# Performance work log

Hardware: AMD Instinct MI355X
Metric: run time of the kernel (lower is better)

The kernel has to match this reference:

```python
import jax, jax.numpy as jnp
import numpy as np

B, S, D_IN, D_OUT, N_EXPERTS = 8, 4096, 512, 512, 8


def setup_inputs() -> dict:
    key = jax.random.key(0)
    k1, k2, k3, k4 = jax.random.split(key, 4)
    x = jax.random.normal(k1, (B, S, D_IN), dtype=jnp.float32)
    partitions = jax.random.randint(k2, (B, S), 0, N_EXPERTS, dtype=jnp.int32)
    # per-branch nn.Linear weights: [n, out_features, in_features], kaiming-ish scale
    W = jax.random.normal(k3, (N_EXPERTS, D_OUT, D_IN), dtype=jnp.float32) * 0.03
    b = jax.random.normal(k4, (N_EXPERTS, D_OUT), dtype=jnp.float32) * 0.01
    return {"x": x, "partitions": partitions, "W": W, "b": b}


def reference(x, partitions, W, b):
    # Hard token partition -> per-branch linear -> scatter combine.
    # Equivalent math to dynamic_partition + branch Linear + dynamic_stitch:
    # out[t] = x[t] @ W[p[t]].T + b[p[t]]
    in_shape = x.shape
    xf = x.reshape(-1, in_shape[-1])          # [T, d_in]
    p = partitions.reshape(-1)                # [T]
    # Compute all-expert outputs, then select per-token expert (vectorized
    # replacement for the variable-size per-partition GEMM loop).
    y = jnp.einsum('td,eod->teo', xf, W) + b[None, :, :]   # [T, n, d_out]
    out = jnp.take_along_axis(y, p[:, None, None], axis=1)[:, 0, :]  # [T, d_out]
    return out.reshape(in_shape[:-1] + (W.shape[1],))
```

## Files before the change

### kernel.cpp

```cpp
#include <hip/hip_runtime.h>
#include <hip/hip_bf16.h>

#define N_EXPERTS 8
#define T_TOKENS 32768
#define D 512
#define TILE 128
#define BK 64
#define NT 4
#define LT_MAX 256
#define GEMM_GRID (N_EXPERTS * LT_MAX * NT)
#define SCATTER_BLOCKS (T_TOKENS / 256)
#define CONVW_BLOCKS ((N_EXPERTS * D * D) / (8 * 256))
#define CONVX_BLOCKS ((T_TOKENS * D) / (8 * 256))

typedef __bf16 bf16x8 __attribute__((ext_vector_type(8)));
typedef float  f32x4  __attribute__((ext_vector_type(4)));
typedef unsigned short u16x8 __attribute__((ext_vector_type(8)));

__device__ __forceinline__ unsigned short f2bf(float f) {
    unsigned int u = __float_as_uint(f);
    u += 0x7FFFu + ((u >> 16) & 1u);
    return (unsigned short)(u >> 16);
}

__device__ __forceinline__ u16x8 cvt8(float4 a, float4 b) {
    u16x8 o;
    o[0] = f2bf(a.x); o[1] = f2bf(a.y); o[2] = f2bf(a.z); o[3] = f2bf(a.w);
    o[4] = f2bf(b.x); o[5] = f2bf(b.y); o[6] = f2bf(b.z); o[7] = f2bf(b.w);
    return o;
}

__device__ __forceinline__ void gl2lds16(const void* g, void* l) {
    __builtin_amdgcn_global_load_lds(
        (const __attribute__((address_space(1))) void*)g,
        (__attribute__((address_space(3))) void*)l, 16, 0, 0);
}

__global__ __launch_bounds__(256) void prep_kernel(
        const int* __restrict__ p, int* __restrict__ fill, int* __restrict__ sorted,
        const float* __restrict__ W, unsigned short* __restrict__ Wb,
        const float* __restrict__ x, unsigned short* __restrict__ xb) {
    int bid = blockIdx.x;
    int tid = threadIdx.x;
    if (bid < SCATTER_BLOCKS) {
        __shared__ int lcount[N_EXPERTS];
        __shared__ int lbase[N_EXPERTS];
        if (tid < N_EXPERTS) lcount[tid] = 0;
        __syncthreads();
        int t = bid * 256 + tid;
        int e = p[t];
        int lrank = atomicAdd(&lcount[e], 1);
        __syncthreads();
        if (tid < N_EXPERTS)
            lbase[tid] = (lcount[tid] > 0) ? atomicAdd(&fill[tid], lcount[tid]) : 0;
        __syncthreads();
        sorted[e * T_TOKENS + (lbase[e] + 1 + lrank)] = t;
    } else if (bid < SCATTER_BLOCKS + CONVW_BLOCKS) {
        size_t i = ((size_t)(bid - SCATTER_BLOCKS) * 256 + tid) * 8;
        float4 a = *(const float4*)(W + i);
        float4 b = *(const float4*)(W + i + 4);
        *(u16x8*)&Wb[i] = cvt8(a, b);
    } else {
        size_t i = ((size_t)(bid - SCATTER_BLOCKS - CONVW_BLOCKS) * 256 + tid) * 8;
        float4 a = *(const float4*)(x + i);
        float4 b = *(const float4*)(x + i + 4);
        *(u16x8*)&xb[i] = cvt8(a, b);
    }
}

__global__ __launch_bounds__(256, 2) void moe_gemm_dma(
        const unsigned short* __restrict__ xb, const unsigned short* __restrict__ Wb,
        const float* __restrict__ bias, const int* __restrict__ fill,
        const int* __restrict__ sorted, float* __restrict__ out) {
    __shared__ int s_idx[TILE];
    __shared__ unsigned short buf[2][2][TILE * BK];

    int bid = blockIdx.x;
    int e = bid & 7;
    int cnt = fill[e] + 1;
    int j = bid >> 3;
    int lt = j >> 2, bn = j & 3;
    int row0 = lt * TILE;
    if (row0 >= cnt) return;

    int tid = threadIdx.x;
    if (tid < TILE) {
        int r = row0 + tid;
        s_idx[tid] = (r < cnt) ? sorted[e * T_TOKENS + r] : -1;
    }
    __syncthreads();

    int wave = tid >> 6, lane = tid & 63;
    int wm = (wave >> 1) * 64, wn = (wave & 1) * 64;
    int lrow = lane & 15, lq = lane >> 4;
    int srow = lane >> 3, scol = lane & 7, swz = scol ^ srow;

    const unsigned short* gA[4];
#pragma unroll
    for (int t = 0; t < 4; t++) {
        int tok = s_idx[wave * 32 + t * 8 + srow];
        gA[t] = xb + (size_t)(tok < 0 ? 0 : tok) * D + swz * 8;
    }
    const unsigned short* gB = Wb + (size_t)e * D * D
                             + (size_t)(bn * TILE + wave * 32 + srow) * D + swz * 8;

#define STAGE(K, KB) do {                                                     \
    _Pragma("unroll") for (int t = 0; t < 4; t++)                             \
        gl2lds16(gA[t] + (K) * BK, &buf[KB][0][(wave * 32 + t * 8) * BK]);    \
    _Pragma("unroll") for (int t = 0; t < 4; t++)                             \
        gl2lds16(gB + (size_t)(t * 8) * D + (K) * BK,                         \
                 &buf[KB][1][(wave * 32 + t * 8) * BK]);                      \
} while (0)

    f32x4 acc[4][4];
#pragma unroll
    for (int i = 0; i < 4; i++)
#pragma unroll
        for (int j2 = 0; j2 < 4; j2++)
            acc[i][j2] = (f32x4){0.f, 0.f, 0.f, 0.f};

    STAGE(0, 0);

#pragma unroll
    for (int step = 0; step < 8; step++) {
        asm volatile("s_waitcnt lgkmcnt(0)" ::: "memory");
        __builtin_amdgcn_s_barrier();
        __builtin_amdgcn_sched_barrier(0);
        if (step < 7) {
            STAGE(step + 1, (step + 1) & 1);
            __builtin_amdgcn_sched_barrier(0);
            asm volatile("s_waitcnt vmcnt(8)" ::: "memory");
        } else {
            asm volatile("s_waitcnt vmcnt(0)" ::: "memory");
        }
        __builtin_amdgcn_s_barrier();
        __builtin_amdgcn_sched_barrier(0);
        const unsigned short* sA = buf[step & 1][0];
        const unsigned short* sB = buf[step & 1][1];
        __builtin_amdgcn_s_setprio(1);
#pragma unroll
        for (int ks = 0; ks < 2; ks++) {
            bf16x8 af[4], bfr[4];
#pragma unroll
            for (int i = 0; i < 4; i++) {
                int row = wm + 16 * i + lrow;
                int cb = (ks * 4 + lq) ^ (lrow & 7);
                af[i] = *(const bf16x8*)&sA[row * BK + cb * 8];
            }
#pragma unroll
            for (int j2 = 0; j2 < 4; j2++) {
                int row = wn + 16 * j2 + lrow;
                int cb = (ks * 4 + lq) ^ (lrow & 7);
                bfr[j2] = *(const bf16x8*)&sB[row * BK + cb * 8];
            }
#pragma unroll
            for (int i = 0; i < 4; i++)
#pragma unroll
                for (int j2 = 0; j2 < 4; j2++)
                    acc[i][j2] = __builtin_amdgcn_mfma_f32_16x16x32_bf16(
                        af[i], bfr[j2], acc[i][j2], 0, 0, 0);
        }
        __builtin_amdgcn_s_setprio(0);
    }
#undef STAGE

#pragma unroll
    for (int j2 = 0; j2 < 4; j2++) {
        float bv = bias[e * D + bn * TILE + wn + 16 * j2 + lrow];
#pragma unroll
        for (int i = 0; i < 4; i++)
#pragma unroll
            for (int r = 0; r < 4; r++)
                acc[i][j2][r] += bv;
    }

    float* ct = (float*)&buf[0][0][0];
#pragma unroll
    for (int p = 0; p < 2; p++) {
        asm volatile("s_waitcnt lgkmcnt(0)" ::: "memory");
        __builtin_amdgcn_s_barrier();
        if ((wave >> 1) == p) {
#pragma unroll
            for (int j2 = 0; j2 < 4; j2++)
#pragma unroll
                for (int i = 0; i < 4; i++)
#pragma unroll
                    for (int r = 0; r < 4; r++)
                        ct[(16 * i + lq * 4 + r) * TILE + wn + 16 * j2 + lrow]
                            = acc[i][j2][r];
        }
        asm volatile("s_waitcnt lgkmcnt(0)" ::: "memory");
        __builtin_amdgcn_s_barrier();
#pragma unroll
        for (int k = 0; k < 8; k++) {
            int u = tid + 256 * k;
            int row = u >> 5, ch = u & 31;
            int tok = s_idx[p * 64 + row];
            f32x4 v = *(const f32x4*)&ct[row * TILE + ch * 4];
            if (tok >= 0)
                *(f32x4*)&out[(size_t)tok * D + bn * TILE + ch * 4] = v;
        }
    }
}

__global__ __launch_bounds__(256) void moe_gemm_f32(
        const float* __restrict__ x, const float* __restrict__ W,
        const float* __restrict__ bias, const int* __restrict__ fill,
        const int* __restrict__ sorted, float* __restrict__ out) {
    __shared__ int s_idx[TILE];
    __shared__ unsigned short sA[TILE][BK + 8];
    __shared__ unsigned short sB[TILE][BK + 8];

    int bid = blockIdx.x;
    int e = bid & 7;
    int cnt = fill[e] + 1;
    int j = bid >> 3;
    int lt = j >> 2, bn = j & 3;
    int row0 = lt * TILE;
    if (row0 >= cnt) return;

    int tid = threadIdx.x;
    if (tid < TILE) {
        int r = row0 + tid;
        s_idx[tid] = (r < cnt) ? sorted[e * T_TOKENS + r] : -1;
    }
    __syncthreads();

    const float* Wbp = W + (size_t)e * D * D + (size_t)(bn * TILE) * D;

    f32x4 acc[4][4];
#pragma unroll
    for (int i = 0; i < 4; i++)
#pragma unroll
        for (int j2 = 0; j2 < 4; j2++)
            acc[i][j2] = (f32x4){0.f, 0.f, 0.f, 0.f};

    int wave = tid >> 6, lane = tid & 63;
    int wm = (wave >> 1) * 64, wn = (wave & 1) * 64;
    int lrow = lane & 15, lq = lane >> 4;

    for (int kk = 0; kk < D; kk += BK) {
#pragma unroll
        for (int i = 0; i < 8; i++) {
            int flat = tid + i * 256;
            int r = flat >> 4, c = (flat & 15) << 2;
            int tok = s_idx[r];
            float4 v = make_float4(0.f, 0.f, 0.f, 0.f);
            if (tok >= 0) v = *(const float4*)(x + (size_t)tok * D + kk + c);
            ushort4 w4;
            w4.x = f2bf(v.x); w4.y = f2bf(v.y); w4.z = f2bf(v.z); w4.w = f2bf(v.w);
            *(ushort4*)&sA[r][c] = w4;
        }
#pragma unroll
        for (int i = 0; i < 8; i++) {
            int flat = tid + i * 256;
            int r = flat >> 4, c = (flat & 15) << 2;
            float4 v = *(const float4*)(Wbp + (size_t)r * D + kk + c);
            ushort4 w4;
            w4.x = f2bf(v.x); w4.y = f2bf(v.y); w4.z = f2bf(v.z); w4.w = f2bf(v.w);
            *(ushort4*)&sB[r][c] = w4;
        }
        __syncthreads();
#pragma unroll
        for (int ks = 0; ks < 2; ks++) {
            bf16x8 af[4], bfr[4];
#pragma unroll
            for (int i = 0; i < 4; i++)
                af[i] = *(const bf16x8*)&sA[wm + 16 * i + lrow][ks * 32 + lq * 8];
#pragma unroll
            for (int j2 = 0; j2 < 4; j2++)
                bfr[j2] = *(const bf16x8*)&sB[wn + 16 * j2 + lrow][ks * 32 + lq * 8];
#pragma unroll
            for (int i = 0; i < 4; i++)
#pragma unroll
                for (int j2 = 0; j2 < 4; j2++)
                    acc[i][j2] = __builtin_amdgcn_mfma_f32_16x16x32_bf16(
                        af[i], bfr[j2], acc[i][j2], 0, 0, 0);
        }
        __syncthreads();
    }

#pragma unroll
    for (int j2 = 0; j2 < 4; j2++) {
        int ng = bn * TILE + wn + 16 * j2 + lrow;
        float bv = bias[e * D + ng];
#pragma unroll
        for (int i = 0; i < 4; i++) {
#pragma unroll
            for (int r = 0; r < 4; r++) {
                int mrow = wm + 16 * i + lq * 4 + r;
                int tok = s_idx[mrow];
                if (tok >= 0)
                    out[(size_t)tok * D + ng] = acc[i][j2][r] + bv;
            }
        }
    }
}

extern "C" void kernel_launch(void* const* d_in, const int* in_sizes, int n_in,
                              void* d_out, int out_size, void* d_ws, size_t ws_size,
                              hipStream_t stream) {
    const float* x    = (const float*)d_in[0];
    const int*   part = (const int*)d_in[1];
    const float* W    = (const float*)d_in[2];
    const float* b    = (const float*)d_in[3];
    float* out = (float*)d_out;

    const size_t xb_elems     = (size_t)T_TOKENS * D;
    const size_t wb_elems     = (size_t)N_EXPERTS * D * D;
    const size_t sorted_elems = (size_t)N_EXPERTS * T_TOKENS;
    const size_t fast_bytes   = (xb_elems + wb_elems) * 2 + (sorted_elems + 8) * 4;
    const size_t slow_bytes   = (sorted_elems + 8) * 4;

    if (ws_size >= fast_bytes) {
        unsigned short* xb = (unsigned short*)d_ws;
        unsigned short* Wb = xb + xb_elems;
        int* sorted = (int*)(Wb + wb_elems);
        int* fill   = sorted + sorted_elems;

        hipMemsetAsync(fill, 0xFF, N_EXPERTS * sizeof(int), stream);
        prep_kernel<<<SCATTER_BLOCKS + CONVW_BLOCKS + CONVX_BLOCKS, 256, 0, stream>>>(
            part, fill, sorted, W, Wb, x, xb);
        moe_gemm_dma<<<GEMM_GRID, 256, 0, stream>>>(xb, Wb, b, fill, sorted, out);
    } else if (ws_size >= slow_bytes) {
        int* sorted = (int*)d_ws;
        int* fill   = sorted + sorted_elems;

        hipMemsetAsync(fill, 0xFF, N_EXPERTS * sizeof(int), stream);
        prep_kernel<<<SCATTER_BLOCKS, 256, 0, stream>>>(
            part, fill, sorted, W, (unsigned short*)nullptr,
            x, (unsigned short*)nullptr);
        moe_gemm_f32<<<GEMM_GRID, 256, 0, stream>>>(x, W, b, fill, sorted, out);
    }
}
```

Before: 153.6 us.

## Use 256x256 GEMM tiles with 512 threads and a compact expert-tile grid

Replaces the 128x128 MoE GEMM kernel with a 256x256-tile version run by 512 threads, with each wave computing a 128x64 sub-tile. The old sparse grid launched every possible expert tile and had most blocks exit early; the new grid is compact, and each block finds its expert and local tile by a prefix scan over per-expert tile counts. Larger tiles raise operand reuse and cut redundant loads of A and B. In exchange the kernel needs about 128KB of LDS, which allows only one block per CU, and its roughly 270 blocks on 256 CUs leave a small tail wave.

```diff
diff --git a/kernel.cpp b/kernel.cpp
--- a/kernel.cpp
+++ b/kernel.cpp
@@ -4,11 +4,14 @@
 #define N_EXPERTS 8
 #define T_TOKENS 32768
 #define D 512
+#define BM 256
+#define BN 256
+#define BK 64
+#define MT_MAX 135
+#define GRID2 (MT_MAX * 2)
 #define TILE 128
-#define BK 64
-#define NT 4
 #define LT_MAX 256
-#define GEMM_GRID (N_EXPERTS * LT_MAX * NT)
+#define GEMM_GRID (N_EXPERTS * LT_MAX * 4)
 #define SCATTER_BLOCKS (T_TOKENS / 256)
 #define CONVW_BLOCKS ((N_EXPERTS * D * D) / (8 * 256))
 #define CONVX_BLOCKS ((T_TOKENS * D) / (8 * 256))
@@ -68,30 +71,38 @@
     }
 }
 
-__global__ __launch_bounds__(256, 2) void moe_gemm_dma(
+__global__ __launch_bounds__(512, 2) void moe_gemm_256(
         const unsigned short* __restrict__ xb, const unsigned short* __restrict__ Wb,
         const float* __restrict__ bias, const int* __restrict__ fill,
         const int* __restrict__ sorted, float* __restrict__ out) {
-    __shared__ int s_idx[TILE];
-    __shared__ unsigned short buf[2][2][TILE * BK];
+    __shared__ int s_idx[BM];
+    __shared__ unsigned short smem[4 * BM * BK];
+    unsigned short* sAb = smem;
+    unsigned short* sBb = smem + 2 * BM * BK;
 
     int bid = blockIdx.x;
-    int e = bid & 7;
-    int cnt = fill[e] + 1;
-    int j = bid >> 3;
-    int lt = j >> 2, bn = j & 3;
-    int row0 = lt * TILE;
-    if (row0 >= cnt) return;
+    int bn = bid & 1, m = bid >> 1;
+
+    int e = 0, lt = 0, tacc = 0, found = 0, cnt_e = 0;
+#pragma unroll
+    for (int i = 0; i < N_EXPERTS; i++) {
+        int c = fill[i] + 1;
+        int tiles = (c + BM - 1) >> 8;
+        if (!found && m < tacc + tiles) { e = i; lt = m - tacc; cnt_e = c; found = 1; }
+        tacc += tiles;
+    }
+    if (!found) return;
+    int row0 = lt * BM;
 
     int tid = threadIdx.x;
-    if (tid < TILE) {
+    if (tid < BM) {
         int r = row0 + tid;
-        s_idx[tid] = (r < cnt) ? sorted[e * T_TOKENS + r] : -1;
+        s_idx[tid] = (r < cnt_e) ? sorted[e * T_TOKENS + r] : -1;
     }
     __syncthreads();
 
     int wave = tid >> 6, lane = tid & 63;
-    int wm = (wave >> 1) * 64, wn = (wave & 1) * 64;
+    int wm = (wave >> 2) * 128, wn = (wave & 3) * 64;
     int lrow = lane & 15, lq = lane >> 4;
     int srow = lane >> 3, scol = lane & 7, swz = scol ^ srow;
 
@@ -102,19 +113,20 @@
         gA[t] = xb + (size_t)(tok < 0 ? 0 : tok) * D + swz * 8;
     }
     const unsigned short* gB = Wb + (size_t)e * D * D
-                             + (size_t)(bn * TILE + wave * 32 + srow) * D + swz * 8;
-
-#define STAGE(K, KB) do {                                                     \
-    _Pragma("unroll") for (int t = 0; t < 4; t++)                             \
-        gl2lds16(gA[t] + (K) * BK, &buf[KB][0][(wave * 32 + t * 8) * BK]);    \
-    _Pragma("unroll") for (int t = 0; t < 4; t++)                             \
-        gl2lds16(gB + (size_t)(t * 8) * D + (K) * BK,                         \
-                 &buf[KB][1][(wave * 32 + t * 8) * BK]);                      \
+                             + (size_t)(bn * BN + wave * 32 + srow) * D + swz * 8;
+
+#define STAGE(K, KB) do {                                                       \
+    _Pragma("unroll") for (int t = 0; t < 4; t++)                               \
+        gl2lds16(gA[t] + (K) * BK,                                              \
+                 &sAb[(KB) * BM * BK + (wave * 32 + t * 8) * BK]);              \
+    _Pragma("unroll") for (int t = 0; t < 4; t++)                               \
+        gl2lds16(gB + (size_t)(t * 8) * D + (K) * BK,                           \
+                 &sBb[(KB) * BM * BK + (wave * 32 + t * 8) * BK]);              \
 } while (0)
 
-    f32x4 acc[4][4];
-#pragma unroll
-    for (int i = 0; i < 4; i++)
+    f32x4 acc[8][4];
+#pragma unroll
+    for (int i = 0; i < 8; i++)
 #pragma unroll
         for (int j2 = 0; j2 < 4; j2++)
             acc[i][j2] = (f32x4){0.f, 0.f, 0.f, 0.f};
@@ -135,26 +147,21 @@
         }
         __builtin_amdgcn_s_barrier();
         __builtin_amdgcn_sched_barrier(0);
-        const unsigned short* sA = buf[step & 1][0];
-        const unsigned short* sB = buf[step & 1][1];
+        const unsigned short* cA = sAb + (step & 1) * BM * BK;
+        const unsigned short* cB = sBb + (step & 1) * BM * BK;
         __builtin_amdgcn_s_setprio(1);
 #pragma unroll
         for (int ks = 0; ks < 2; ks++) {
-            bf16x8 af[4], bfr[4];
-#pragma unroll
-            for (int i = 0; i < 4; i++) {
-                int row = wm + 16 * i + lrow;
-                int cb = (ks * 4 + lq) ^ (lrow & 7);
-                af[i] = *(const bf16x8*)&sA[row * BK + cb * 8];
-            }
-#pragma unroll
-            for (int j2 = 0; j2 < 4; j2++) {
-                int row = wn + 16 * j2 + lrow;
-                int cb = (ks * 4 + lq) ^ (lrow & 7);
-                bfr[j2] = *(const bf16x8*)&sB[row * BK + cb * 8];
-            }
-#pragma unroll
-            for (int i = 0; i < 4; i++)
+            int cb = (ks * 4 + lq) ^ (lrow & 7);
+            bf16x8 af[8], bfr[4];
+#pragma unroll
+            for (int i = 0; i < 8; i++)
+                af[i] = *(const bf16x8*)&cA[(wm + 16 * i + lrow) * BK + cb * 8];
+#pragma unroll
+            for (int j2 = 0; j2 < 4; j2++)
+                bfr[j2] = *(const bf16x8*)&cB[(wn + 16 * j2 + lrow) * BK + cb * 8];
+#pragma unroll
+            for (int i = 0; i < 8; i++)
 #pragma unroll
                 for (int j2 = 0; j2 < 4; j2++)
                     acc[i][j2] = __builtin_amdgcn_mfma_f32_16x16x32_bf16(
@@ -166,39 +173,39 @@
 
 #pragma unroll
     for (int j2 = 0; j2 < 4; j2++) {
-        float bv = bias[e * D + bn * TILE + wn + 16 * j2 + lrow];
-#pragma unroll
-        for (int i = 0; i < 4; i++)
+        float bv = bias[e * D + bn * BN + wn + 16 * j2 + lrow];
+#pragma unroll
+        for (int i = 0; i < 8; i++)
 #pragma unroll
             for (int r = 0; r < 4; r++)
                 acc[i][j2][r] += bv;
     }
 
-    float* ct = (float*)&buf[0][0][0];
+    float* ct = (float*)smem;
 #pragma unroll
     for (int p = 0; p < 2; p++) {
         asm volatile("s_waitcnt lgkmcnt(0)" ::: "memory");
         __builtin_amdgcn_s_barrier();
-        if ((wave >> 1) == p) {
-#pragma unroll
-            for (int j2 = 0; j2 < 4; j2++)
-#pragma unroll
-                for (int i = 0; i < 4; i++)
+        if ((wave >> 2) == p) {
+#pragma unroll
+            for (int i = 0; i < 8; i++)
+#pragma unroll
+                for (int j2 = 0; j2 < 4; j2++)
 #pragma unroll
                     for (int r = 0; r < 4; r++)
-                        ct[(16 * i + lq * 4 + r) * TILE + wn + 16 * j2 + lrow]
+                        ct[(16 * i + lq * 4 + r) * BN + wn + 16 * j2 + lrow]
                             = acc[i][j2][r];
         }
         asm volatile("s_waitcnt lgkmcnt(0)" ::: "memory");
         __builtin_amdgcn_s_barrier();
 #pragma unroll
-        for (int k = 0; k < 8; k++) {
-            int u = tid + 256 * k;
-            int row = u >> 5, ch = u & 31;
-            int tok = s_idx[p * 64 + row];
-            f32x4 v = *(const f32x4*)&ct[row * TILE + ch * 4];
+        for (int k = 0; k < 16; k++) {
+            int u = tid + 512 * k;
+            int row = u >> 6, ch = u & 63;
+            int tok = s_idx[p * 128 + row];
+            f32x4 v = *(const f32x4*)&ct[row * BN + ch * 4];
             if (tok >= 0)
-                *(f32x4*)&out[(size_t)tok * D + bn * TILE + ch * 4] = v;
+                *(f32x4*)&out[(size_t)tok * D + bn * BN + ch * 4] = v;
         }
     }
 }
@@ -321,7 +328,7 @@
         hipMemsetAsync(fill, 0xFF, N_EXPERTS * sizeof(int), stream);
         prep_kernel<<<SCATTER_BLOCKS + CONVW_BLOCKS + CONVX_BLOCKS, 256, 0, stream>>>(
             part, fill, sorted, W, Wb, x, xb);
-        moe_gemm_dma<<<GEMM_GRID, 256, 0, stream>>>(xb, Wb, b, fill, sorted, out);
+        moe_gemm_256<<<GRID2, 512, 0, stream>>>(xb, Wb, b, fill, sorted, out);
     } else if (ws_size >= slow_bytes) {
         int* sorted = (int*)d_ws;
         int* fill   = sorted + sorted_elems;
```

Result: slower. 162.4 us (+5.7%).

## Pre-gather tokens into packed swizzled bf16 tiles and compact the GEMM grid

Applied to the files above, without the earlier changes.

Input conversion now happens per expert tile. A new gather kernel reads the sorted token indices and writes each 128-row tile of x as bf16, contiguous and pre-swizzled per K chunk. W is likewise converted into per-(expert, column-block) packed swizzled tiles. The GEMM streams both operands with fully contiguous global-to-LDS loads, and its grid covers only the occupied tiles through a prefix walk over the expert counts, instead of launching 8x256x4 blocks that mostly exit early. The cost is an extra kernel launch and a serial dependency on the scatter result before gathering.

```diff
diff --git a/kernel.cpp b/kernel.cpp
--- a/kernel.cpp
+++ b/kernel.cpp
@@ -6,12 +6,15 @@
 #define D 512
 #define TILE 128
 #define BK 64
-#define NT 4
+#define NKK (D / BK)
+#define CHUNK 8192
+#define TILE_U16 (NKK * CHUNK)
+#define MT_MAX 264
+#define GRID_WG (MT_MAX * 4)
+#define SCATTER_BLOCKS (T_TOKENS / 256)
+#define CONVW_BLOCKS 128
 #define LT_MAX 256
-#define GEMM_GRID (N_EXPERTS * LT_MAX * NT)
-#define SCATTER_BLOCKS (T_TOKENS / 256)
-#define CONVW_BLOCKS ((N_EXPERTS * D * D) / (8 * 256))
-#define CONVX_BLOCKS ((T_TOKENS * D) / (8 * 256))
+#define GEMM_GRID (N_EXPERTS * LT_MAX * 4)
 
 typedef __bf16 bf16x8 __attribute__((ext_vector_type(8)));
 typedef float  f32x4  __attribute__((ext_vector_type(4)));
@@ -36,10 +39,9 @@
         (__attribute__((address_space(3))) void*)l, 16, 0, 0);
 }
 
-__global__ __launch_bounds__(256) void prep_kernel(
+__global__ __launch_bounds__(256) void scatter_convw(
         const int* __restrict__ p, int* __restrict__ fill, int* __restrict__ sorted,
-        const float* __restrict__ W, unsigned short* __restrict__ Wb,
-        const float* __restrict__ x, unsigned short* __restrict__ xb) {
+        const float* __restrict__ W, unsigned short* __restrict__ Wt) {
     int bid = blockIdx.x;
     int tid = threadIdx.x;
     if (bid < SCATTER_BLOCKS) {
@@ -55,61 +57,102 @@
             lbase[tid] = (lcount[tid] > 0) ? atomicAdd(&fill[tid], lcount[tid]) : 0;
         __syncthreads();
         sorted[e * T_TOKENS + (lbase[e] + 1 + lrank)] = t;
-    } else if (bid < SCATTER_BLOCKS + CONVW_BLOCKS) {
-        size_t i = ((size_t)(bid - SCATTER_BLOCKS) * 256 + tid) * 8;
-        float4 a = *(const float4*)(W + i);
-        float4 b = *(const float4*)(W + i + 4);
-        *(u16x8*)&Wb[i] = cvt8(a, b);
     } else {
-        size_t i = ((size_t)(bid - SCATTER_BLOCKS - CONVW_BLOCKS) * 256 + tid) * 8;
-        float4 a = *(const float4*)(x + i);
-        float4 b = *(const float4*)(x + i + 4);
-        *(u16x8*)&xb[i] = cvt8(a, b);
-    }
-}
-
-__global__ __launch_bounds__(256, 2) void moe_gemm_dma(
-        const unsigned short* __restrict__ xb, const unsigned short* __restrict__ Wb,
+        int i2 = bid - SCATTER_BLOCKS;
+        int e = i2 >> 4, bn = (i2 >> 2) & 3, q = i2 & 3;
+        int wave = tid >> 6, lane = tid & 63;
+        int kk = lane >> 3, b = lane & 7;
+        unsigned short* base = Wt + (size_t)(e * 4 + bn) * TILE_U16 + kk * CHUNK;
+#pragma unroll
+        for (int rr = 0; rr < 8; rr++) {
+            int row = q * 32 + wave * 8 + rr;
+            const float* src = W + ((size_t)e * D + bn * TILE + row) * D + lane * 8;
+            float4 a = *(const float4*)src;
+            float4 c = *(const float4*)(src + 4);
+            *(u16x8*)&base[row * 64 + ((b ^ (row & 7)) << 3)] = cvt8(a, c);
+        }
+    }
+}
+
+__global__ __launch_bounds__(256) void gather_pack_x(
+        const float* __restrict__ x, const int* __restrict__ fill,
+        const int* __restrict__ sorted, unsigned short* __restrict__ xs) {
+    int m = blockIdx.x;
+    int e = 0, lt = 0, tacc = 0, found = 0, cnt_e = 0;
+#pragma unroll
+    for (int i = 0; i < N_EXPERTS; i++) {
+        int c = fill[i] + 1;
+        int tiles = (c + TILE - 1) >> 7;
+        if (!found && m < tacc + tiles) { e = i; lt = m - tacc; cnt_e = c; found = 1; }
+        tacc += tiles;
+    }
+    if (!found) return;
+
+    int tid = threadIdx.x, wave = tid >> 6, lane = tid & 63;
+    int kk = lane >> 3, b = lane & 7;
+    unsigned short* base = xs + (size_t)m * TILE_U16 + kk * CHUNK;
+    int row0 = lt * TILE;
+#pragma unroll 4
+    for (int rr = 0; rr < 32; rr++) {
+        int row = wave * 32 + rr;
+        int r = row0 + row;
+        int tok = (r < cnt_e) ? sorted[e * T_TOKENS + r] : -1;
+        u16x8 v = (u16x8)0;
+        if (tok >= 0) {
+            const float* src = x + (size_t)tok * D + lane * 8;
+            float4 a = *(const float4*)src;
+            float4 c = *(const float4*)(src + 4);
+            v = cvt8(a, c);
+        }
+        *(u16x8*)&base[row * 64 + ((b ^ (row & 7)) << 3)] = v;
+    }
+}
+
+__global__ __launch_bounds__(256, 2) void moe_gemm_pk(
+        const unsigned short* __restrict__ xs, const unsigned short* __restrict__ Wt,
         const float* __restrict__ bias, const int* __restrict__ fill,
         const int* __restrict__ sorted, float* __restrict__ out) {
     __shared__ int s_idx[TILE];
-    __shared__ unsigned short buf[2][2][TILE * BK];
+    __shared__ unsigned short sA[2][TILE * BK];
+    __shared__ unsigned short sB[2][TILE * BK];
 
     int bid = blockIdx.x;
-    int e = bid & 7;
-    int cnt = fill[e] + 1;
-    int j = bid >> 3;
-    int lt = j >> 2, bn = j & 3;
+    int w6 = bid >> 3;
+    int m = (bid & 7) + (w6 >> 2) * 8;
+    int bn = w6 & 3;
+
+    int e = 0, lt = 0, tacc = 0, found = 0, cnt_e = 0;
+#pragma unroll
+    for (int i = 0; i < N_EXPERTS; i++) {
+        int c = fill[i] + 1;
+        int tiles = (c + TILE - 1) >> 7;
+        if (!found && m < tacc + tiles) { e = i; lt = m - tacc; cnt_e = c; found = 1; }
+        tacc += tiles;
+    }
+    if (!found) return;
     int row0 = lt * TILE;
-    if (row0 >= cnt) return;
 
     int tid = threadIdx.x;
     if (tid < TILE) {
         int r = row0 + tid;
-        s_idx[tid] = (r < cnt) ? sorted[e * T_TOKENS + r] : -1;
+        s_idx[tid] = (r < cnt_e) ? sorted[e * T_TOKENS + r] : -1;
     }
     __syncthreads();
 
     int wave = tid >> 6, lane = tid & 63;
     int wm = (wave >> 1) * 64, wn = (wave & 1) * 64;
     int lrow = lane & 15, lq = lane >> 4;
-    int srow = lane >> 3, scol = lane & 7, swz = scol ^ srow;
-
-    const unsigned short* gA[4];
-#pragma unroll
-    for (int t = 0; t < 4; t++) {
-        int tok = s_idx[wave * 32 + t * 8 + srow];
-        gA[t] = xb + (size_t)(tok < 0 ? 0 : tok) * D + swz * 8;
-    }
-    const unsigned short* gB = Wb + (size_t)e * D * D
-                             + (size_t)(bn * TILE + wave * 32 + srow) * D + swz * 8;
-
-#define STAGE(K, KB) do {                                                     \
-    _Pragma("unroll") for (int t = 0; t < 4; t++)                             \
-        gl2lds16(gA[t] + (K) * BK, &buf[KB][0][(wave * 32 + t * 8) * BK]);    \
-    _Pragma("unroll") for (int t = 0; t < 4; t++)                             \
-        gl2lds16(gB + (size_t)(t * 8) * D + (K) * BK,                         \
-                 &buf[KB][1][(wave * 32 + t * 8) * BK]);                      \
+
+    const unsigned short* gAc = xs + (size_t)m * TILE_U16;
+    const unsigned short* gBc = Wt + (size_t)(e * 4 + bn) * TILE_U16;
+
+#define STAGE(K, KB) do {                                                      \
+    _Pragma("unroll") for (int t = 0; t < 4; t++)                              \
+        gl2lds16(gAc + (size_t)(K) * CHUNK + (wave * 4 + t) * 512 + lane * 8,  \
+                 &sA[KB][(wave * 4 + t) * 512]);                               \
+    _Pragma("unroll") for (int t = 0; t < 4; t++)                              \
+        gl2lds16(gBc + (size_t)(K) * CHUNK + (wave * 4 + t) * 512 + lane * 8,  \
+                 &sB[KB][(wave * 4 + t) * 512]);                               \
 } while (0)
 
     f32x4 acc[4][4];
@@ -122,11 +165,11 @@
     STAGE(0, 0);
 
 #pragma unroll
-    for (int step = 0; step < 8; step++) {
+    for (int step = 0; step < NKK; step++) {
         asm volatile("s_waitcnt lgkmcnt(0)" ::: "memory");
         __builtin_amdgcn_s_barrier();
         __builtin_amdgcn_sched_barrier(0);
-        if (step < 7) {
+        if (step < NKK - 1) {
             STAGE(step + 1, (step + 1) & 1);
             __builtin_amdgcn_sched_barrier(0);
             asm volatile("s_waitcnt vmcnt(8)" ::: "memory");
@@ -135,24 +178,19 @@
         }
         __builtin_amdgcn_s_barrier();
         __builtin_amdgcn_sched_barrier(0);
-        const unsigned short* sA = buf[step & 1][0];
-        const unsigned short* sB = buf[step & 1][1];
+        const unsigned short* cA = sA[step & 1];
+        const unsigned short* cB = sB[step & 1];
         __builtin_amdgcn_s_setprio(1);
 #pragma unroll
         for (int ks = 0; ks < 2; ks++) {
+            int cb = (ks * 4 + lq) ^ (lrow & 7);
             bf16x8 af[4], bfr[4];
 #pragma unroll
-            for (int i = 0; i < 4; i++) {
-                int row = wm + 16 * i + lrow;
-                int cb = (ks * 4 + lq) ^ (lrow & 7);
-                af[i] = *(const bf16x8*)&sA[row * BK + cb * 8];
-            }
-#pragma unroll
-            for (int j2 = 0; j2 < 4; j2++) {
-                int row = wn + 16 * j2 + lrow;
-                int cb = (ks * 4 + lq) ^ (lrow & 7);
-                bfr[j2] = *(const bf16x8*)&sB[row * BK + cb * 8];
-            }
+            for (int i = 0; i < 4; i++)
+                af[i] = *(const bf16x8*)&cA[(wm + 16 * i + lrow) * BK + cb * 8];
+#pragma unroll
+            for (int j2 = 0; j2 < 4; j2++)
+                bfr[j2] = *(const bf16x8*)&cB[(wn + 16 * j2 + lrow) * BK + cb * 8];
 #pragma unroll
             for (int i = 0; i < 4; i++)
 #pragma unroll
@@ -174,16 +212,16 @@
                 acc[i][j2][r] += bv;
     }
 
-    float* ct = (float*)&buf[0][0][0];
+    float* ct = (float*)&sA[0][0];
 #pragma unroll
     for (int p = 0; p < 2; p++) {
         asm volatile("s_waitcnt lgkmcnt(0)" ::: "memory");
         __builtin_amdgcn_s_barrier();
         if ((wave >> 1) == p) {
 #pragma unroll
-            for (int j2 = 0; j2 < 4; j2++)
-#pragma unroll
-                for (int i = 0; i < 4; i++)
+            for (int i = 0; i < 4; i++)
+#pragma unroll
+                for (int j2 = 0; j2 < 4; j2++)
 #pragma unroll
                     for (int r = 0; r < 4; r++)
                         ct[(16 * i + lq * 4 + r) * TILE + wn + 16 * j2 + lrow]
@@ -306,30 +344,30 @@
     const float* b    = (const float*)d_in[3];
     float* out = (float*)d_out;
 
-    const size_t xb_elems     = (size_t)T_TOKENS * D;
-    const size_t wb_elems     = (size_t)N_EXPERTS * D * D;
+    const size_t xs_elems     = (size_t)MT_MAX * TILE_U16;
+    const size_t wt_elems     = (size_t)N_EXPERTS * 4 * TILE_U16;
     const size_t sorted_elems = (size_t)N_EXPERTS * T_TOKENS;
-    const size_t fast_bytes   = (xb_elems + wb_elems) * 2 + (sorted_elems + 8) * 4;
+    const size_t fast_bytes   = (xs_elems + wt_elems) * 2 + (sorted_elems + 8) * 4;
     const size_t slow_bytes   = (sorted_elems + 8) * 4;
 
     if (ws_size >= fast_bytes) {
-        unsigned short* xb = (unsigned short*)d_ws;
-        unsigned short* Wb = xb + xb_elems;
-        int* sorted = (int*)(Wb + wb_elems);
+        unsigned short* xs = (unsigned short*)d_ws;
+        unsigned short* Wt = xs + xs_elems;
+        int* sorted = (int*)(Wt + wt_elems);
         int* fill   = sorted + sorted_elems;
 
         hipMemsetAsync(fill, 0xFF, N_EXPERTS * sizeof(int), stream);
-        prep_kernel<<<SCATTER_BLOCKS + CONVW_BLOCKS + CONVX_BLOCKS, 256, 0, stream>>>(
-            part, fill, sorted, W, Wb, x, xb);
-        moe_gemm_dma<<<GEMM_GRID, 256, 0, stream>>>(xb, Wb, b, fill, sorted, out);
+        scatter_convw<<<SCATTER_BLOCKS + CONVW_BLOCKS, 256, 0, stream>>>(
+            part, fill, sorted, W, Wt);
+        gather_pack_x<<<MT_MAX, 256, 0, stream>>>(x, fill, sorted, xs);
+        moe_gemm_pk<<<GRID_WG, 256, 0, stream>>>(xs, Wt, b, fill, sorted, out);
     } else if (ws_size >= slow_bytes) {
         int* sorted = (int*)d_ws;
         int* fill   = sorted + sorted_elems;
 
         hipMemsetAsync(fill, 0xFF, N_EXPERTS * sizeof(int), stream);
-        prep_kernel<<<SCATTER_BLOCKS, 256, 0, stream>>>(
-            part, fill, sorted, W, (unsigned short*)nullptr,
-            x, (unsigned short*)nullptr);
+        scatter_convw<<<SCATTER_BLOCKS, 256, 0, stream>>>(
+            part, fill, sorted, (const float*)nullptr, (unsigned short*)nullptr);
         moe_gemm_f32<<<GEMM_GRID, 256, 0, stream>>>(x, W, b, fill, sorted, out);
     }
 }
```

Measured after the change: 190.9 us. 1.24x slower.
